# Performance work log

Hardware: AMD Instinct MI355X
Metric: run time of the kernel (lower is better)

Reference implementation:

```python
import jax, jax.numpy as jnp
import numpy as np

D_MODEL = 1024
N_HEAD = 16


def setup_inputs() -> dict:
    key = jax.random.key(0)
    ks = jax.random.split(key, 12)
    B, S, D = 4, 2048, D_MODEL
    scale = 1.0 / np.sqrt(D)
    inp = {
        "Q": jax.random.normal(ks[0], (B, S, D), jnp.float32),
        "K": jax.random.normal(ks[1], (B, S, D), jnp.float32),
        "V": jax.random.normal(ks[2], (B, S, D), jnp.float32),
        "Wq": jax.random.normal(ks[3], (D, D), jnp.float32) * scale,
        "bq": jax.random.normal(ks[4], (D,), jnp.float32) * scale,
        "Wk": jax.random.normal(ks[5], (D, D), jnp.float32) * scale,
        "bk": jax.random.normal(ks[6], (D,), jnp.float32) * scale,
        "Wv": jax.random.normal(ks[7], (D, D), jnp.float32) * scale,
        "bv": jax.random.normal(ks[8], (D,), jnp.float32) * scale,
        "Wo": jax.random.normal(ks[9], (D, D), jnp.float32) * scale,
        "bo": jax.random.normal(ks[10], (D,), jnp.float32) * scale,
    }
    return inp


def _split_heads(x, n_head):
    B, S, D = x.shape
    return x.reshape(B, S, n_head, D // n_head).transpose(0, 2, 1, 3)  # [B,H,S,dh]


def reference(Q, K, V, Wq, bq, Wk, bk, Wv, bv, Wo, bo):
    # torch Linear: x @ W.T + b
    q = _split_heads(Q @ Wq.T + bq, N_HEAD)
    k = _split_heads(K @ Wk.T + bk, N_HEAD)
    v = _split_heads(V @ Wv.T + bv, N_HEAD)
    d_k = k.shape[-1]
    score = jnp.einsum('bhqd,bhkd->bhqk', q, k) / jnp.sqrt(jnp.float32(d_k))
    attn = jax.nn.softmax(score, axis=-1)
    out = jnp.einsum('bhqk,bhkd->bhqd', attn, v)  # [B,H,S,dh]
    B, H, S, dh = out.shape
    out = out.transpose(0, 2, 1, 3).reshape(B, S, H * dh)
    return out @ Wo.T + bo
```

## Files before the change

### kernel.cpp

```cpp
#include <hip/hip_runtime.h>
#include <math.h>

#define D_MODEL 1024
#define N_HEAD  16
#define DH      64
#define SEQ     2048
#define BATCH   4
#define BH      (BATCH*N_HEAD)
#define MROWS   (BATCH*SEQ)

typedef __attribute__((ext_vector_type(8)))  short          s16x8;
typedef __attribute__((ext_vector_type(8)))  unsigned short u16x8;
typedef __attribute__((ext_vector_type(4)))  unsigned short u16x4;
typedef __attribute__((ext_vector_type(4)))  float          f32x4;
typedef __attribute__((ext_vector_type(16))) float          f32x16;
typedef __attribute__((ext_vector_type(4)))  unsigned int   u32x4;

#define QSCALE 0.18033688f

__device__ __forceinline__ unsigned short f2bf(float x) {
    unsigned int u = __float_as_uint(x);
    u += 0x7FFFu + ((u >> 16) & 1u);
    return (unsigned short)(u >> 16);
}

__device__ __forceinline__ unsigned int cvtpk_bf16(float lo, float hi) {
    unsigned int r;
    asm("v_cvt_pk_bf16_f32 %0, %1, %2" : "=v"(r) : "v"(lo), "v"(hi));
    return r;
}

__device__ __forceinline__ float exp2_asm(float x) {
    float r;
    asm("v_exp_f32 %0, %1" : "=v"(r) : "v"(x));
    return r;
}

__global__ __launch_bounds__(256) void conv_w4(const float* __restrict__ w0,
                                               const float* __restrict__ w1,
                                               const float* __restrict__ w2,
                                               const float* __restrict__ w3,
                                               unsigned short* __restrict__ o0,
                                               unsigned short* __restrict__ o1,
                                               unsigned short* __restrict__ o2,
                                               unsigned short* __restrict__ o3)
{
    const float* w; unsigned short* o;
    switch (blockIdx.y) {
        case 0:  w = w0; o = o0; break;
        case 1:  w = w1; o = o1; break;
        case 2:  w = w2; o = o2; break;
        default: w = w3; o = o3; break;
    }
    int i = blockIdx.x * 256 + threadIdx.x;
    const float4* p = (const float4*)w + (size_t)i * 2;
    float4 a = p[0], b = p[1];
    u16x8 v;
    v[0] = f2bf(a.x); v[1] = f2bf(a.y); v[2] = f2bf(a.z); v[3] = f2bf(a.w);
    v[4] = f2bf(b.x); v[5] = f2bf(b.y); v[6] = f2bf(b.z); v[7] = f2bf(b.w);
    *((u16x8*)o + i) = v;
}

template<int MODE, bool AF32>
__global__ __launch_bounds__(256) void gemm_bt(const void* __restrict__ Av,
                                               const unsigned short* __restrict__ W,
                                               const float* __restrict__ bias,
                                               unsigned short* __restrict__ outb,
                                               float* __restrict__ outf,
                                               float oscale)
{
    __shared__ short As[128 * 64];
    __shared__ short Bs[128 * 64];
    const int tid = threadIdx.x;
    const int w = tid >> 6, l = tid & 63;
    const int lr = l & 15, lg = l >> 4;
    const int wm = w >> 1, wn = w & 1;
    const int r0 = blockIdx.x * 128, c0 = blockIdx.y * 128;
    const int srow = tid >> 3;
    const int sc8  = tid & 7;

    f32x4 zz = {0.f, 0.f, 0.f, 0.f};
    f32x4 acc[4][4];
    #pragma unroll
    for (int i = 0; i < 4; ++i)
        #pragma unroll
        for (int j = 0; j < 4; ++j) acc[i][j] = zz;

    const unsigned short* Ab = (const unsigned short*)Av;
    const float*          Af = (const float*)Av;

    u16x8 ar[4], br[4];
    float4 arf[4][2];
    #pragma unroll
    for (int p = 0; p < 4; ++p) {
        int row = p * 32 + srow;
        if (AF32) {
            arf[p][0] = *(const float4*)(Af + (size_t)(r0 + row) * 1024 + sc8 * 8);
            arf[p][1] = *(const float4*)(Af + (size_t)(r0 + row) * 1024 + sc8 * 8 + 4);
        } else {
            ar[p] = *(const u16x8*)(Ab + (size_t)(r0 + row) * 1024 + sc8 * 8);
        }
        br[p] = *(const u16x8*)(W + (size_t)(c0 + row) * 1024 + sc8 * 8);
    }

    for (int ks = 0; ks < 16; ++ks) {
        __syncthreads();
        #pragma unroll
        for (int p = 0; p < 4; ++p) {
            int row = p * 32 + srow;
            if (AF32) {
                u32x4 wd;
                wd[0] = cvtpk_bf16(arf[p][0].x, arf[p][0].y);
                wd[1] = cvtpk_bf16(arf[p][0].z, arf[p][0].w);
                wd[2] = cvtpk_bf16(arf[p][1].x, arf[p][1].y);
                wd[3] = cvtpk_bf16(arf[p][1].z, arf[p][1].w);
                *(u16x8*)&As[row * 64 + ((sc8 ^ (row & 7)) * 8)] = __builtin_bit_cast(u16x8, wd);
            } else {
                *(u16x8*)&As[row * 64 + ((sc8 ^ (row & 7)) * 8)] = ar[p];
            }
            *(u16x8*)&Bs[row * 64 + ((sc8 ^ (row & 7)) * 8)] = br[p];
        }
        __syncthreads();
        if (ks < 15) {
            int k0 = (ks + 1) * 64;
            #pragma unroll
            for (int p = 0; p < 4; ++p) {
                int row = p * 32 + srow;
                if (AF32) {
                    arf[p][0] = *(const float4*)(Af + (size_t)(r0 + row) * 1024 + k0 + sc8 * 8);
                    arf[p][1] = *(const float4*)(Af + (size_t)(r0 + row) * 1024 + k0 + sc8 * 8 + 4);
                } else {
                    ar[p] = *(const u16x8*)(Ab + (size_t)(r0 + row) * 1024 + k0 + sc8 * 8);
                }
                br[p] = *(const u16x8*)(W + (size_t)(c0 + row) * 1024 + k0 + sc8 * 8);
            }
        }
        #pragma unroll
        for (int t = 0; t < 2; ++t) {
            const int k8 = lg + 4 * t;
            s16x8 af[4], bw[4];
            #pragma unroll
            for (int i = 0; i < 4; ++i) {
                int rowa = wm * 64 + i * 16 + lr;
                af[i] = *(const s16x8*)&As[rowa * 64 + ((k8 ^ (rowa & 7)) * 8)];
                int rowb = wn * 64 + i * 16 + lr;
                bw[i] = *(const s16x8*)&Bs[rowb * 64 + ((k8 ^ (rowb & 7)) * 8)];
            }
            #pragma unroll
            for (int i = 0; i < 4; ++i)
                #pragma unroll
                for (int j = 0; j < 4; ++j)
                    acc[i][j] = __builtin_amdgcn_mfma_f32_16x16x32_bf16(af[i], bw[j], acc[i][j], 0, 0, 0);
        }
    }

    #pragma unroll
    for (int i = 0; i < 4; ++i) {
        #pragma unroll
        for (int j = 0; j < 4; ++j) {
            const int colb = c0 + wn * 64 + j * 16 + lr;
            const float bv = bias[colb];
            if (MODE == 2) {
                const int row = r0 + wm * 64 + i * 16 + lg * 4;
                const int b = row >> 11, s = row & 2047;
                const int h = colb >> 6, d = colb & 63;
                u16x4 pv;
                pv[0] = f2bf((acc[i][j][0] + bv) * oscale);
                pv[1] = f2bf((acc[i][j][1] + bv) * oscale);
                pv[2] = f2bf((acc[i][j][2] + bv) * oscale);
                pv[3] = f2bf((acc[i][j][3] + bv) * oscale);
                *(u16x4*)(outb + ((size_t)(b * N_HEAD + h) * DH + d) * SEQ + s) = pv;
            } else {
                #pragma unroll
                for (int rg = 0; rg < 4; ++rg) {
                    const int row = r0 + wm * 64 + i * 16 + lg * 4 + rg;
                    const float v = acc[i][j][rg] + bv;
                    if (MODE == 0) {
                        outf[(size_t)row * D_MODEL + colb] = v;
                    } else {
                        const int b = row >> 11, s = row & 2047;
                        const int h = colb >> 6, d = colb & 63;
                        outb[((size_t)(b * N_HEAD + h) * SEQ + s) * DH + d] = f2bf(v * oscale);
                    }
                }
            }
        }
    }
}

__global__ __launch_bounds__(256, 4) void flash_attn_mfma32(const unsigned short* __restrict__ qb,
                                                            const unsigned short* __restrict__ kb,
                                                            const unsigned short* __restrict__ vtb,
                                                            unsigned short* __restrict__ aob)
{
    __shared__ u16x8 Kt[2][512];
    __shared__ u16x8 Vt[2][512];

    const int tid = threadIdx.x;
    const int w = tid >> 6, l = tid & 63;
    const int q32 = l & 31;
    const int h = l >> 5;

    const int wg   = blockIdx.x;
    const int xcd  = wg & 7;
    const int slot = wg >> 3;
    const int bh   = xcd * 8 + (slot >> 4);
    const int qt   = slot & 15;

    const unsigned short* qh = qb + (size_t)bh * SEQ * DH;
    const unsigned short* kh = kb + (size_t)bh * SEQ * DH;
    const unsigned short* vh = vtb + (size_t)bh * DH * SEQ;

    const int qrow = qt * 128 + w * 32 + q32;

    s16x8 qf[4];
    #pragma unroll
    for (int ks = 0; ks < 4; ++ks)
        qf[ks] = *(const s16x8*)(qh + (size_t)qrow * DH + ks * 16 + h * 8);

    f32x16 O[2];
    #pragma unroll
    for (int c = 0; c < 2; ++c)
        #pragma unroll
        for (int r = 0; r < 16; ++r) O[c][r] = 0.f;
    float m = 0.f, lsum = 0.f;

    const int srow = tid >> 3;
    const int sc8  = tid & 7;

    u16x8 kreg[2], vreg[2];
    #pragma unroll
    for (int p = 0; p < 2; ++p) {
        int rr = p * 32 + srow;
        kreg[p] = *(const u16x8*)(kh + (size_t)rr * DH + sc8 * 8);
        vreg[p] = *(const u16x8*)(vh + (size_t)rr * SEQ + sc8 * 8);
    }
    #pragma unroll
    for (int p = 0; p < 2; ++p) {
        int rr = p * 32 + srow;
        Kt[0][sc8 * 64 + (rr ^ sc8)] = kreg[p];
        Vt[0][sc8 * 64 + (rr ^ sc8)] = vreg[p];
    }
    __syncthreads();

    int buf = 0;
    for (int kv = 0; kv < SEQ / 64; ++kv) {
        if (kv < SEQ / 64 - 1) {
            const int s0 = (kv + 1) * 64;
            #pragma unroll
            for (int p = 0; p < 2; ++p) {
                int rr = p * 32 + srow;
                kreg[p] = *(const u16x8*)(kh + (size_t)(s0 + rr) * DH + sc8 * 8);
                vreg[p] = *(const u16x8*)(vh + (size_t)rr * SEQ + s0 + sc8 * 8);
            }
        }

        f32x16 seed;
        #pragma unroll
        for (int r = 0; r < 16; ++r) seed[r] = -m;
        f32x16 SC[2];
        SC[0] = seed; SC[1] = seed;
        __builtin_amdgcn_s_setprio(1);
        #pragma unroll
        for (int ks = 0; ks < 4; ++ks) {
            const int chunk = 2 * ks + h;
            #pragma unroll
            for (int c = 0; c < 2; ++c) {
                const int row = c * 32 + q32;
                s16x8 kf = __builtin_bit_cast(s16x8, Kt[buf][chunk * 64 + (row ^ chunk)]);
                SC[c] = __builtin_amdgcn_mfma_f32_32x32x16_bf16(kf, qf[ks], SC[c], 0, 0, 0);
            }
        }
        __builtin_amdgcn_s_setprio(0);

        float t0[8];
        #pragma unroll
        for (int r = 0; r < 8; ++r)
            t0[r] = fmaxf(fmaxf(fmaxf(SC[0][r], SC[0][r + 8]), SC[1][r]), SC[1][r + 8]);
        #pragma unroll
        for (int d = 4; d; d >>= 1)
            #pragma unroll
            for (int r = 0; r < d; ++r) t0[r] = fmaxf(t0[r], t0[r + d]);
        float rmb = fmaxf(t0[0], __shfl_xor(t0[0], 32, 64));

        if (!__all(rmb <= 8.0f)) {
            const float delta = fmaxf(rmb, 0.f);
            const float fold = exp2_asm(-delta);
            lsum *= fold;
            O[0] *= fold;
            O[1] *= fold;
            m += delta;
            #pragma unroll
            for (int c = 0; c < 2; ++c)
                #pragma unroll
                for (int r = 0; r < 16; ++r)
                    SC[c][r] -= delta;
        }

        #pragma unroll
        for (int c = 0; c < 2; ++c)
            #pragma unroll
            for (int r = 0; r < 16; ++r)
                SC[c][r] = exp2_asm(SC[c][r]);

        float s0a[8];
        #pragma unroll
        for (int r = 0; r < 8; ++r)
            s0a[r] = (SC[0][r] + SC[0][r + 8]) + (SC[1][r] + SC[1][r + 8]);
        #pragma unroll
        for (int d = 4; d; d >>= 1)
            #pragma unroll
            for (int r = 0; r < d; ++r) s0a[r] += s0a[r + d];
        lsum += s0a[0] + __shfl_xor(s0a[0], 32, 64);

        s16x8 pa[4];
        #pragma unroll
        for (int s = 0; s < 4; ++s) {
            const int c = s >> 1, rb = (s & 1) * 8;
            unsigned int a0 = cvtpk_bf16(SC[c][rb + 0], SC[c][rb + 1]);
            unsigned int a1 = cvtpk_bf16(SC[c][rb + 2], SC[c][rb + 3]);
            unsigned int b0 = cvtpk_bf16(SC[c][rb + 4], SC[c][rb + 5]);
            unsigned int b1 = cvtpk_bf16(SC[c][rb + 6], SC[c][rb + 7]);
            unsigned int x0 = (unsigned int)__shfl_xor((int)a0, 32, 64);
            unsigned int x1 = (unsigned int)__shfl_xor((int)a1, 32, 64);
            unsigned int y0 = (unsigned int)__shfl_xor((int)b0, 32, 64);
            unsigned int y1 = (unsigned int)__shfl_xor((int)b1, 32, 64);
            u32x4 wd;
            wd[0] = h ? y0 : a0;
            wd[1] = h ? y1 : a1;
            wd[2] = h ? b0 : x0;
            wd[3] = h ? b1 : x1;
            pa[s] = __builtin_bit_cast(s16x8, wd);
        }

        __builtin_amdgcn_s_setprio(1);
        #pragma unroll
        for (int s = 0; s < 4; ++s) {
            const int chunk = 2 * s + h;
            #pragma unroll
            for (int c = 0; c < 2; ++c) {
                const int row = c * 32 + q32;
                s16x8 vf = __builtin_bit_cast(s16x8, Vt[buf][chunk * 64 + (row ^ chunk)]);
                O[c] = __builtin_amdgcn_mfma_f32_32x32x16_bf16(vf, pa[s], O[c], 0, 0, 0);
            }
        }
        __builtin_amdgcn_s_setprio(0);

        if (kv < SEQ / 64 - 1) {
            #pragma unroll
            for (int p = 0; p < 2; ++p) {
                int rr = p * 32 + srow;
                Kt[buf ^ 1][sc8 * 64 + (rr ^ sc8)] = kreg[p];
                Vt[buf ^ 1][sc8 * 64 + (rr ^ sc8)] = vreg[p];
            }
            __syncthreads();
            buf ^= 1;
        }
    }

    const float inv = 1.0f / lsum;
    const int b = bh >> 4, head = bh & 15;
    unsigned short* obase = aob + ((size_t)b * SEQ + qrow) * D_MODEL + head * DH;
    #pragma unroll
    for (int c = 0; c < 2; ++c) {
        #pragma unroll
        for (int rq = 0; rq < 4; ++rq) {
            const int d0 = 8 * rq + 4 * h + 32 * c;
            u16x4 pv;
            #pragma unroll
            for (int j = 0; j < 4; ++j) pv[j] = f2bf(O[c][rq * 4 + j] * inv);
            *(u16x4*)(obase + d0) = pv;
        }
    }
}

extern "C" void kernel_launch(void* const* d_in, const int* in_sizes, int n_in,
                              void* d_out, int out_size, void* d_ws, size_t ws_size,
                              hipStream_t stream)
{
    const float* Q  = (const float*)d_in[0];
    const float* K  = (const float*)d_in[1];
    const float* V  = (const float*)d_in[2];
    const float* Wq = (const float*)d_in[3];
    const float* bq = (const float*)d_in[4];
    const float* Wk = (const float*)d_in[5];
    const float* bk = (const float*)d_in[6];
    const float* Wv = (const float*)d_in[7];
    const float* bv = (const float*)d_in[8];
    const float* Wo = (const float*)d_in[9];
    const float* bo = (const float*)d_in[10];

    const size_t PER = (size_t)MROWS * D_MODEL;
    const size_t WSZ = (size_t)D_MODEL * D_MODEL;
    unsigned short* wqb = (unsigned short*)d_ws;
    unsigned short* wkb = wqb + WSZ;
    unsigned short* wvb = wkb + WSZ;
    unsigned short* wob = wvb + WSZ;
    unsigned short* qb2 = wob + WSZ;
    unsigned short* kb2 = qb2 + PER;
    unsigned short* vtb = kb2 + PER;
    unsigned short* aob = vtb + PER;

    dim3 gg(MROWS / 128, D_MODEL / 128);

    conv_w4<<<dim3(512, 4), 256, 0, stream>>>(Wq, Wk, Wv, Wo, wqb, wkb, wvb, wob);

    gemm_bt<1, true><<<gg, 256, 0, stream>>>(Q, wqb, bq, qb2, nullptr, QSCALE);
    gemm_bt<1, true><<<gg, 256, 0, stream>>>(K, wkb, bk, kb2, nullptr, 1.0f);
    gemm_bt<2, true><<<gg, 256, 0, stream>>>(V, wvb, bv, vtb, nullptr, 1.0f);

    flash_attn_mfma32<<<dim3(16 * BH), 256, 0, stream>>>(qb2, kb2, vtb, aob);

    gemm_bt<0, false><<<gg, 256, 0, stream>>>(aob, wob, bo, nullptr, (float*)d_out, 1.0f);
}
```

Measured before the change: 227.4 us.

## Load K/V tiles directly into LDS and compute row sums with MFMA

Replaces the register-staged K/V prefetch (global load into VGPRs, then ds_write) with global_load_lds direct-to-LDS transfers, keeping the XOR swizzle through per-lane source offsets. The softmax row sum is no longer a VALU reduction with a cross-lane shuffle; an extra MFMA against a ones vector accumulates it into a 32x32 accumulator, and the row max now uses v_max3. This is meant to cut VGPR pressure and VALU/LDS-write work in the attention loop. In exchange it adds 16 accumulator registers and one extra MFMA per k-step, and it depends on the async LDS load being complete at the barrier.

Result: slower. 247.4 us (+8.8%).

```diff
diff --git a/kernel.cpp b/kernel.cpp
--- a/kernel.cpp
+++ b/kernel.cpp
@@ -18,6 +18,10 @@
 
 #define QSCALE 0.18033688f
 
+typedef const __attribute__((address_space(1))) unsigned int gu32;
+typedef __attribute__((address_space(3))) unsigned int lu32;
+#define GLOAD_LDS16(g, l) __builtin_amdgcn_global_load_lds((gu32*)(g), (lu32*)(l), 16, 0, 0)
+
 __device__ __forceinline__ unsigned short f2bf(float x) {
     unsigned int u = __float_as_uint(x);
     u += 0x7FFFu + ((u >> 16) & 1u);
@@ -33,6 +37,12 @@
 __device__ __forceinline__ float exp2_asm(float x) {
     float r;
     asm("v_exp_f32 %0, %1" : "=v"(r) : "v"(x));
+    return r;
+}
+
+__device__ __forceinline__ float max3f(float a, float b, float c) {
+    float r;
+    asm("v_max3_f32 %0, %1, %2, %3" : "=v"(r) : "v"(a), "v"(b), "v"(c));
     return r;
 }
 
@@ -208,8 +218,8 @@
     const int qt   = slot & 15;
 
     const unsigned short* qh = qb + (size_t)bh * SEQ * DH;
-    const unsigned short* kh = kb + (size_t)bh * SEQ * DH;
-    const unsigned short* vh = vtb + (size_t)bh * DH * SEQ;
+    const char* kptr = (const char*)(kb + (size_t)bh * SEQ * DH);
+    const char* vptr = (const char*)(vtb + (size_t)bh * DH * SEQ);
 
     const int qrow = qt * 128 + w * 32 + q32;
 
@@ -218,48 +228,47 @@
     for (int ks = 0; ks < 4; ++ks)
         qf[ks] = *(const s16x8*)(qh + (size_t)qrow * DH + ks * 16 + h * 8);
 
-    f32x16 O[2];
-    #pragma unroll
-    for (int c = 0; c < 2; ++c)
-        #pragma unroll
-        for (int r = 0; r < 16; ++r) O[c][r] = 0.f;
-    float m = 0.f, lsum = 0.f;
-
-    const int srow = tid >> 3;
-    const int sc8  = tid & 7;
-
-    u16x8 kreg[2], vreg[2];
+    f32x16 O[2], Ls;
+    #pragma unroll
+    for (int r = 0; r < 16; ++r) { O[0][r] = 0.f; O[1][r] = 0.f; Ls[r] = 0.f; }
+    float m = 0.f;
+
+    u16x8 onesv;
+    #pragma unroll
+    for (int r = 0; r < 8; ++r) onesv[r] = 0x3F80;
+    const s16x8 ones = __builtin_bit_cast(s16x8, onesv);
+
+    size_t koff[2], voff[2];
     #pragma unroll
     for (int p = 0; p < 2; ++p) {
-        int rr = p * 32 + srow;
-        kreg[p] = *(const u16x8*)(kh + (size_t)rr * DH + sc8 * 8);
-        vreg[p] = *(const u16x8*)(vh + (size_t)rr * SEQ + sc8 * 8);
-    }
+        const int chunk = 2 * w + p;
+        const int rowp = l ^ chunk;
+        koff[p] = (size_t)rowp * (DH * 2) + chunk * 16;
+        voff[p] = (size_t)rowp * (SEQ * 2) + chunk * 16;
+    }
+
     #pragma unroll
     for (int p = 0; p < 2; ++p) {
-        int rr = p * 32 + srow;
-        Kt[0][sc8 * 64 + (rr ^ sc8)] = kreg[p];
-        Vt[0][sc8 * 64 + (rr ^ sc8)] = vreg[p];
+        const int chunk = 2 * w + p;
+        GLOAD_LDS16(kptr + koff[p], &Kt[0][chunk * 64]);
+        GLOAD_LDS16(vptr + voff[p], &Vt[0][chunk * 64]);
     }
     __syncthreads();
 
     int buf = 0;
     for (int kv = 0; kv < SEQ / 64; ++kv) {
         if (kv < SEQ / 64 - 1) {
-            const int s0 = (kv + 1) * 64;
             #pragma unroll
             for (int p = 0; p < 2; ++p) {
-                int rr = p * 32 + srow;
-                kreg[p] = *(const u16x8*)(kh + (size_t)(s0 + rr) * DH + sc8 * 8);
-                vreg[p] = *(const u16x8*)(vh + (size_t)rr * SEQ + s0 + sc8 * 8);
-            }
-        }
-
-        f32x16 seed;
-        #pragma unroll
-        for (int r = 0; r < 16; ++r) seed[r] = -m;
+                const int chunk = 2 * w + p;
+                GLOAD_LDS16(kptr + (size_t)(kv + 1) * (64 * DH * 2) + koff[p], &Kt[buf ^ 1][chunk * 64]);
+                GLOAD_LDS16(vptr + (size_t)(kv + 1) * 128 + voff[p], &Vt[buf ^ 1][chunk * 64]);
+            }
+        }
+
         f32x16 SC[2];
-        SC[0] = seed; SC[1] = seed;
+        #pragma unroll
+        for (int r = 0; r < 16; ++r) { SC[0][r] = -m; SC[1][r] = -m; }
         __builtin_amdgcn_s_setprio(1);
         #pragma unroll
         for (int ks = 0; ks < 4; ++ks) {
@@ -273,20 +282,24 @@
         }
         __builtin_amdgcn_s_setprio(0);
 
-        float t0[8];
-        #pragma unroll
-        for (int r = 0; r < 8; ++r)
-            t0[r] = fmaxf(fmaxf(fmaxf(SC[0][r], SC[0][r + 8]), SC[1][r]), SC[1][r + 8]);
-        #pragma unroll
-        for (int d = 4; d; d >>= 1)
-            #pragma unroll
-            for (int r = 0; r < d; ++r) t0[r] = fmaxf(t0[r], t0[r + d]);
-        float rmb = fmaxf(t0[0], __shfl_xor(t0[0], 32, 64));
+        #define GETSC(i) ((i) < 16 ? SC[0][(i)] : SC[1][(i) - 16])
+        float t0[11];
+        #pragma unroll
+        for (int r = 0; r < 10; ++r)
+            t0[r] = max3f(GETSC(3 * r), GETSC(3 * r + 1), GETSC(3 * r + 2));
+        t0[10] = fmaxf(GETSC(30), GETSC(31));
+        float u0 = max3f(t0[0], t0[1], t0[2]);
+        float u1 = max3f(t0[3], t0[4], t0[5]);
+        float u2 = max3f(t0[6], t0[7], t0[8]);
+        float u3 = fmaxf(t0[9], t0[10]);
+        float rmb_l = fmaxf(max3f(u0, u1, u2), u3);
+        float rmb = fmaxf(rmb_l, __shfl_xor(rmb_l, 32, 64));
+        #undef GETSC
 
         if (!__all(rmb <= 8.0f)) {
             const float delta = fmaxf(rmb, 0.f);
             const float fold = exp2_asm(-delta);
-            lsum *= fold;
+            Ls *= fold;
             O[0] *= fold;
             O[1] *= fold;
             m += delta;
@@ -302,16 +315,6 @@
             #pragma unroll
             for (int r = 0; r < 16; ++r)
                 SC[c][r] = exp2_asm(SC[c][r]);
-
-        float s0a[8];
-        #pragma unroll
-        for (int r = 0; r < 8; ++r)
-            s0a[r] = (SC[0][r] + SC[0][r + 8]) + (SC[1][r] + SC[1][r + 8]);
-        #pragma unroll
-        for (int d = 4; d; d >>= 1)
-            #pragma unroll
-            for (int r = 0; r < d; ++r) s0a[r] += s0a[r + d];
-        lsum += s0a[0] + __shfl_xor(s0a[0], 32, 64);
 
         s16x8 pa[4];
         #pragma unroll
@@ -343,22 +346,17 @@
                 s16x8 vf = __builtin_bit_cast(s16x8, Vt[buf][chunk * 64 + (row ^ chunk)]);
                 O[c] = __builtin_amdgcn_mfma_f32_32x32x16_bf16(vf, pa[s], O[c], 0, 0, 0);
             }
+            Ls = __builtin_amdgcn_mfma_f32_32x32x16_bf16(ones, pa[s], Ls, 0, 0, 0);
         }
         __builtin_amdgcn_s_setprio(0);
 
         if (kv < SEQ / 64 - 1) {
-            #pragma unroll
-            for (int p = 0; p < 2; ++p) {
-                int rr = p * 32 + srow;
-                Kt[buf ^ 1][sc8 * 64 + (rr ^ sc8)] = kreg[p];
-                Vt[buf ^ 1][sc8 * 64 + (rr ^ sc8)] = vreg[p];
-            }
             __syncthreads();
             buf ^= 1;
         }
     }
 
-    const float inv = 1.0f / lsum;
+    const float inv = 1.0f / Ls[0];
     const int b = bh >> 4, head = bh & 15;
     unsigned short* obase = aob + ((size_t)b * SEQ + qrow) * D_MODEL + head * DH;
     #pragma unroll
```
